# Kernel tuning notes

Measured on AMD Instinct MI355X. Metric: run time of the kernel, lower is better.

Reference implementation:

```python
import jax, jax.numpy as jnp
import numpy as np

B, S, D, F, E, K = 4, 2048, 768, 3072, 8, 2
LB_W, Z_W = 0.01, 0.001


def setup_inputs() -> dict:
    key = jax.random.key(0)
    ks = jax.random.split(key, 6)
    x = jax.random.normal(ks[0], (B, S, D), dtype=jnp.float32)
    Wr = jax.random.truncated_normal(ks[1], -2.0, 2.0, (D, E), dtype=jnp.float32) * 0.02
    W1 = jax.random.normal(ks[2], (E, D, F), dtype=jnp.float32) * (1.0 / np.sqrt(D))
    b1 = jnp.zeros((E, F), dtype=jnp.float32)
    W2 = jax.random.normal(ks[3], (E, F, D), dtype=jnp.float32) * (1.0 / np.sqrt(F))
    b2 = jnp.zeros((E, D), dtype=jnp.float32)
    return {"x": x, "Wr": Wr, "W1": W1, "b1": b1, "W2": W2, "b2": b2}


def reference(x, Wr, W1, b1, W2, b2):
    # Router
    router_logits = jnp.einsum('bsd,de->bse', x, Wr)            # [B,S,E]
    router_probs = jax.nn.softmax(router_logits, axis=-1)
    top_k_probs, top_k_idx = jax.lax.top_k(router_probs, K)     # [B,S,K]
    top_k_probs = top_k_probs / (jnp.sum(top_k_probs, axis=-1, keepdims=True) + 1e-8)

    # Auxiliary losses
    expert_usage = jnp.mean(router_probs, axis=(0, 1))          # [E]
    mean_usage = jnp.mean(expert_usage)
    var_usage = jnp.mean(jnp.square(expert_usage - mean_usage))
    lb_loss = var_usage / (mean_usage * mean_usage + 1e-8) * jnp.float32(E)
    z_loss = jnp.mean(jnp.square(jax.nn.logsumexp(router_logits, axis=-1)))

    # Combine weights per expert: sum over top-k slots assigned to expert e
    one_hot = jax.nn.one_hot(top_k_idx, E, dtype=x.dtype)       # [B,S,K,E]
    combine = jnp.sum(one_hot * top_k_probs[..., None], axis=2) # [B,S,E]

    # Expert FFNs (loop over fixed small E, vectorized over tokens)
    output = jnp.zeros_like(x)
    for e in range(E):
        h = jax.nn.gelu(jnp.einsum('bsd,df->bsf', x, W1[e]) + b1[e], approximate=False)
        y = jnp.einsum('bsf,fd->bsd', h, W2[e]) + b2[e]
        output = output + y * combine[..., e:e + 1]

    aux = {"load_balancing_loss": lb_loss * LB_W, "router_z_loss": z_loss * Z_W}
    return output, aux["load_balancing_loss"], aux["router_z_loss"]
```

## Files before the change

kernel.cpp:

```cpp
#include <hip/hip_runtime.h>
#include <cstdint>
#include <cstddef>

#define B_ 4
#define S_ 2048
#define D_ 768
#define F_ 3072
#define E_ 8
#define NTOK (B_*S_)
#define NASSIGN (NTOK*2)
#define RBLK 256
#define FBLK 32
#define MAXTILE 136

typedef unsigned short u16;
typedef __attribute__((ext_vector_type(8))) __bf16 bf16x8;
typedef __attribute__((ext_vector_type(4))) float f32x4;

__device__ __forceinline__ u16 f2bf(float f) {
    unsigned int u = __builtin_bit_cast(unsigned int, f);
    u += 0x7fffu + ((u >> 16) & 1u);
    return (u16)(u >> 16);
}

__device__ __forceinline__ void async16(const void* g, void* l) {
    __builtin_amdgcn_global_load_lds(
        (const __attribute__((address_space(1))) unsigned int*)g,
        (__attribute__((address_space(3))) unsigned int*)l, 16, 0, 0);
}

__device__ __forceinline__ float gelu_f(float v) {
    float z = v * 0.70710678f;
    float a = fabsf(z);
    float t = __builtin_amdgcn_rcpf(1.0f + 0.3275911f * a);
    float poly = t * (0.254829592f + t * (-0.284496736f + t * (1.421413741f +
                 t * (-1.453152027f + t * 1.061405429f))));
    float e = __expf(-z * z);
    float erf_z = copysignf(1.0f - poly * e, z);
    return 0.5f * v * (1.0f + erf_z);
}

__global__ void k_init(int* cursors) {
    int t = threadIdx.x;
    if (t < E_) cursors[t] = 0;
}

__global__ void k_cvt_x(const float* __restrict__ x, u16* __restrict__ xb) {
    int id = blockIdx.x * 256 + threadIdx.x;
    float4 v = ((const float4*)x)[id];
    ushort4 o;
    o.x = f2bf(v.x); o.y = f2bf(v.y); o.z = f2bf(v.z); o.w = f2bf(v.w);
    ((ushort4*)xb)[id] = o;
}

__global__ void k_tcvt(const float* __restrict__ in, u16* __restrict__ out, int R, int C) {
    __shared__ u16 t[32][33];
    int e = blockIdx.z;
    int c0 = blockIdx.x * 32, r0 = blockIdx.y * 32;
    int tx = threadIdx.x & 7;
    int ty = threadIdx.x >> 3;
    const float* ip = in + (size_t)e * R * C + (size_t)(r0 + ty) * C + c0 + tx * 4;
    float4 v = *(const float4*)ip;
    t[tx * 4 + 0][ty] = f2bf(v.x);
    t[tx * 4 + 1][ty] = f2bf(v.y);
    t[tx * 4 + 2][ty] = f2bf(v.z);
    t[tx * 4 + 3][ty] = f2bf(v.w);
    __syncthreads();
    u16* op = out + (size_t)e * C * R + (size_t)(c0 + ty) * R + r0 + tx * 4;
    ushort4 o;
    o.x = t[ty][tx * 4 + 0]; o.y = t[ty][tx * 4 + 1];
    o.z = t[ty][tx * 4 + 2]; o.w = t[ty][tx * 4 + 3];
    *(ushort4*)op = o;
}

__global__ __launch_bounds__(256) void k_router(
    const float* __restrict__ x, const float* __restrict__ Wr,
    float* __restrict__ usage_part, float* __restrict__ z_part,
    int* __restrict__ hist_part,
    int* __restrict__ tk_idx, float* __restrict__ tk_w)
{
    __shared__ float wrt[E_ * D_];
    __shared__ float s_usage[E_];
    __shared__ float s_z;
    __shared__ int   s_hist[E_];
    int tid = threadIdx.x;
    for (int i = tid; i < E_ * D_; i += 256) {
        int d = i >> 3, e = i & 7;
        wrt[e * D_ + d] = Wr[i];
    }
    if (tid < E_) { s_usage[tid] = 0.f; s_hist[tid] = 0; }
    if (tid == 0) s_z = 0.f;
    __syncthreads();

    int w = tid >> 6, lane = tid & 63;
    float u_acc[E_];
    #pragma unroll
    for (int e = 0; e < E_; e++) u_acc[e] = 0.f;
    float z_acc = 0.f;

    for (int it = 0; it < 8; it++) {
        int tok = blockIdx.x * 32 + it * 4 + w;
        float acc[E_];
        #pragma unroll
        for (int e = 0; e < E_; e++) acc[e] = 0.f;
        const float* xr = x + (size_t)tok * D_;
        for (int d = lane; d < D_; d += 64) {
            float xv = xr[d];
            #pragma unroll
            for (int e = 0; e < E_; e++) acc[e] += xv * wrt[e * D_ + d];
        }
        #pragma unroll
        for (int off = 32; off > 0; off >>= 1) {
            #pragma unroll
            for (int e = 0; e < E_; e++) acc[e] += __shfl_down(acc[e], off);
        }
        if (lane == 0) {
            float m = acc[0];
            #pragma unroll
            for (int e = 1; e < E_; e++) m = fmaxf(m, acc[e]);
            float p[E_], s = 0.f;
            #pragma unroll
            for (int e = 0; e < E_; e++) { p[e] = expf(acc[e] - m); s += p[e]; }
            float inv = 1.f / s;
            #pragma unroll
            for (int e = 0; e < E_; e++) { p[e] *= inv; u_acc[e] += p[e]; }
            float lse = m + logf(s);
            z_acc += lse * lse;
            int i1 = 0;
            for (int e = 1; e < E_; e++) if (p[e] > p[i1]) i1 = e;
            int i2 = -1;
            for (int e = 0; e < E_; e++) {
                if (e == i1) continue;
                if (i2 < 0 || p[e] > p[i2]) i2 = e;
            }
            float denom = p[i1] + p[i2] + 1e-8f;
            tk_idx[tok * 2 + 0] = i1; tk_idx[tok * 2 + 1] = i2;
            tk_w[tok * 2 + 0] = p[i1] / denom;
            tk_w[tok * 2 + 1] = p[i2] / denom;
            atomicAdd(&s_hist[i1], 1); atomicAdd(&s_hist[i2], 1);
        }
    }
    if (lane == 0) {
        #pragma unroll
        for (int e = 0; e < E_; e++) atomicAdd(&s_usage[e], u_acc[e]);
        atomicAdd(&s_z, z_acc);
    }
    __syncthreads();
    if (tid < E_) {
        usage_part[blockIdx.x * E_ + tid] = s_usage[tid];
        hist_part[blockIdx.x * E_ + tid]  = s_hist[tid];
    }
    if (tid == 0) z_part[blockIdx.x] = s_z;
}

__global__ __launch_bounds__(256) void k_finalize(
    const float* __restrict__ usage_part, const float* __restrict__ z_part,
    const int* __restrict__ hist_part,
    int* __restrict__ counts, int* __restrict__ offsets,
    int* __restrict__ tile_list,
    float* __restrict__ out_scalars)
{
    __shared__ float s_u[E_];
    __shared__ float s_z;
    __shared__ int   s_h[E_];
    int tid = threadIdx.x;
    if (tid < E_) { s_u[tid] = 0.f; s_h[tid] = 0; }
    if (tid == 0) s_z = 0.f;
    __syncthreads();

    float u[E_]; int h[E_];
    #pragma unroll
    for (int e = 0; e < E_; e++) { u[e] = usage_part[tid * E_ + e]; h[e] = hist_part[tid * E_ + e]; }
    float z = z_part[tid];
    #pragma unroll
    for (int off = 32; off > 0; off >>= 1) {
        #pragma unroll
        for (int e = 0; e < E_; e++) {
            u[e] += __shfl_down(u[e], off);
            h[e] += __shfl_down(h[e], off);
        }
        z += __shfl_down(z, off);
    }
    if ((tid & 63) == 0) {
        #pragma unroll
        for (int e = 0; e < E_; e++) { atomicAdd(&s_u[e], u[e]); atomicAdd(&s_h[e], h[e]); }
        atomicAdd(&s_z, z);
    }
    __syncthreads();
    if (tid == 0) {
        int o = 0, nt = 0;
        for (int e = 0; e < E_; e++) {
            int c = s_h[e];
            counts[e] = c; offsets[e] = o; o += c;
            for (int m0 = 0; m0 < c; m0 += 128) tile_list[1 + nt++] = (m0 << 8) | e;
        }
        tile_list[0] = nt;
        float uu[E_], mean = 0.f;
        for (int e = 0; e < E_; e++) { uu[e] = s_u[e] / (float)NTOK; mean += uu[e]; }
        mean /= (float)E_;
        float var = 0.f;
        for (int e = 0; e < E_; e++) { float d = uu[e] - mean; var += d * d; }
        var /= (float)E_;
        out_scalars[0] = var / (mean * mean + 1e-8f) * (float)E_ * 0.01f;
        out_scalars[1] = (s_z / (float)NTOK) * 0.001f;
    }
}

__global__ __launch_bounds__(256) void k_fill(
    const int* __restrict__ tk_idx, const float* __restrict__ tk_w,
    const int* __restrict__ offsets, int* __restrict__ cursors,
    int* __restrict__ assign_token, float* __restrict__ assign_weight)
{
    __shared__ int l_cnt[E_];
    __shared__ int l_base[E_];
    int tid = threadIdx.x;
    if (tid < E_) l_cnt[tid] = 0;
    __syncthreads();
    int t = blockIdx.x * 256 + tid;
    int e0 = tk_idx[t * 2 + 0], e1 = tk_idx[t * 2 + 1];
    int r0 = atomicAdd(&l_cnt[e0], 1);
    int r1 = atomicAdd(&l_cnt[e1], 1);
    __syncthreads();
    if (tid < E_) l_base[tid] = atomicAdd(&cursors[tid], l_cnt[tid]);
    __syncthreads();
    int row0 = offsets[e0] + l_base[e0] + r0;
    int row1 = offsets[e1] + l_base[e1] + r1;
    assign_token[row0] = t; assign_weight[row0] = tk_w[t * 2 + 0];
    assign_token[row1] = t; assign_weight[row1] = tk_w[t * 2 + 1];
}

__global__ __launch_bounds__(256) void k_gemm1(
    const u16* __restrict__ xb, const u16* __restrict__ w1t,
    const float* __restrict__ b1,
    const int* __restrict__ counts, const int* __restrict__ offsets,
    const int* __restrict__ tile_list,
    const int* __restrict__ assign_token, u16* __restrict__ h)
{
    int bid = blockIdx.x;
    int xcd = bid & 7;
    int j = bid >> 3;
    int nx = j / 17;
    int mt = xcd * 17 + (j % 17);
    int nt = tile_list[0];
    if (mt >= nt) return;
    int packed = tile_list[1 + mt];
    int e = packed & 0xff;
    int m0 = packed >> 8;
    int cnt = counts[e];
    int off = offsets[e];
    int n0 = nx * 128;

    __shared__ __align__(16) u16 SM[16384];
    char* smb = (char*)SM;

    int tid = threadIdx.x;
    int w = tid >> 6, lane = tid & 63;
    int rA = lane >> 2;
    int colk = ((lane & 3) ^ (rA & 3)) * 8;
    int r0 = (w * 2 + 0) * 16 + rA;
    int r1 = (w * 2 + 1) * 16 + rA;

    int c0b = __builtin_amdgcn_readfirstlane((w * 2 + 0) * 1024);
    int c1b = __builtin_amdgcn_readfirstlane((w * 2 + 1) * 1024);

    int g0 = m0 + r0; if (g0 > cnt - 1) g0 = cnt - 1;
    int g1 = m0 + r1; if (g1 > cnt - 1) g1 = cnt - 1;
    const u16* agp0 = xb + (size_t)assign_token[off + g0] * D_ + colk;
    const u16* agp1 = xb + (size_t)assign_token[off + g1] * D_ + colk;
    const u16* bgp0 = w1t + ((size_t)e * F_ + n0 + r0) * D_ + colk;
    const u16* bgp1 = w1t + ((size_t)e * F_ + n0 + r1) * D_ + colk;

    f32x4 acc[4][4];
    #pragma unroll
    for (int i = 0; i < 4; i++)
        #pragma unroll
        for (int j2 = 0; j2 < 4; j2++) acc[i][j2] = (f32x4){0.f, 0.f, 0.f, 0.f};

    int wm = (w >> 1) * 64, wn = (w & 1) * 64;
    int fm = lane & 15;
    int slot = ((lane >> 4) ^ (fm & 3)) * 8;

    #define STAGE1(buf, kk) do { \
        async16(agp0 + (kk), smb + (buf) * 8192 + c0b); \
        async16(agp1 + (kk), smb + (buf) * 8192 + c1b); \
        async16(bgp0 + (kk), smb + 16384 + (buf) * 8192 + c0b); \
        async16(bgp1 + (kk), smb + 16384 + (buf) * 8192 + c1b); \
    } while (0)
    #define COMPUTE1(buf) do { \
        const u16* Ab = SM + (buf) * 4096; \
        const u16* Bb = SM + 8192 + (buf) * 4096; \
        bf16x8 af[4], bfr[4]; \
        _Pragma("unroll") \
        for (int i = 0; i < 4; i++) af[i] = *(const bf16x8*)&Ab[(wm + i * 16 + fm) * 32 + slot]; \
        _Pragma("unroll") \
        for (int j2 = 0; j2 < 4; j2++) bfr[j2] = *(const bf16x8*)&Bb[(wn + j2 * 16 + fm) * 32 + slot]; \
        _Pragma("unroll") \
        for (int i = 0; i < 4; i++) \
            _Pragma("unroll") \
            for (int j2 = 0; j2 < 4; j2++) \
                acc[i][j2] = __builtin_amdgcn_mfma_f32_16x16x32_bf16(af[i], bfr[j2], acc[i][j2], 0, 0, 0); \
    } while (0)

    STAGE1(0, 0);
    __syncthreads();
    for (int kk = 0; kk < D_; kk += 64) {
        STAGE1(1, kk + 32);
        COMPUTE1(0);
        __syncthreads();
        if (kk + 64 < D_) STAGE1(0, kk + 64);
        COMPUTE1(1);
        __syncthreads();
    }
    #undef STAGE1
    #undef COMPUTE1

    int rbase = (lane >> 4) * 4;
    u16* tb = SM + w * 4096;
    float biasv[4];
    #pragma unroll
    for (int j2 = 0; j2 < 4; j2++) biasv[j2] = b1[e * F_ + n0 + wn + j2 * 16 + fm];
    #pragma unroll
    for (int i = 0; i < 4; i++)
        #pragma unroll
        for (int j2 = 0; j2 < 4; j2++)
            #pragma unroll
            for (int r = 0; r < 4; r++) {
                int m_l = i * 16 + rbase + r;
                int f_l = j2 * 16 + fm;
                u16 q = f2bf(gelu_f(acc[i][j2][r] + biasv[j2]));
                tb[m_l * 64 + ((((f_l >> 3) ^ (m_l & 7)) << 3) | (f_l & 7))] = q;
            }
    __syncthreads();
    #pragma unroll
    for (int s = 0; s < 8; s++) {
        int m_l = s * 8 + (lane >> 3);
        int c = lane & 7;
        uint4 vv = *(const uint4*)&tb[m_l * 64 + ((c ^ (m_l & 7)) << 3)];
        int m = m0 + wm + m_l;
        if (m < cnt)
            *(uint4*)&h[(size_t)(off + m) * F_ + n0 + wn + c * 8] = vv;
    }
}

__global__ __launch_bounds__(256) void k_gemm2(
    const u16* __restrict__ h, const u16* __restrict__ w2t,
    const float* __restrict__ b2,
    const int* __restrict__ counts, const int* __restrict__ offsets,
    const int* __restrict__ tile_list,
    const int* __restrict__ assign_token, const float* __restrict__ assign_weight,
    float* __restrict__ out)
{
    int bid = blockIdx.x;
    int xcd = bid & 7;
    int j = bid >> 3;
    int nx = j % 6;
    int mt = xcd * 17 + (j / 6);
    int nt = tile_list[0];
    if (mt >= nt) return;
    int packed = tile_list[1 + mt];
    int e = packed & 0xff;
    int m0 = packed >> 8;
    int cnt = counts[e];
    int off = offsets[e];
    int n0 = nx * 128;

    __shared__ __align__(16) u16 SM[16384];
    char* smb = (char*)SM;

    int tid = threadIdx.x;
    int w = tid >> 6, lane = tid & 63;
    int rA = lane >> 2;
    int colk = ((lane & 3) ^ (rA & 3)) * 8;
    int r0 = (w * 2 + 0) * 16 + rA;
    int r1 = (w * 2 + 1) * 16 + rA;

    int c0b = __builtin_amdgcn_readfirstlane((w * 2 + 0) * 1024);
    int c1b = __builtin_amdgcn_readfirstlane((w * 2 + 1) * 1024);

    const u16* agp0 = h + (size_t)(off + m0 + r0) * F_ + colk;
    const u16* agp1 = h + (size_t)(off + m0 + r1) * F_ + colk;
    const u16* bgp0 = w2t + ((size_t)e * D_ + n0 + r0) * F_ + colk;
    const u16* bgp1 = w2t + ((size_t)e * D_ + n0 + r1) * F_ + colk;

    f32x4 acc[4][4];
    #pragma unroll
    for (int i = 0; i < 4; i++)
        #pragma unroll
        for (int j2 = 0; j2 < 4; j2++) acc[i][j2] = (f32x4){0.f, 0.f, 0.f, 0.f};

    int wm = (w >> 1) * 64, wn = (w & 1) * 64;
    int fm = lane & 15;
    int slot = ((lane >> 4) ^ (fm & 3)) * 8;

    #define STAGE2(buf, kk) do { \
        async16(agp0 + (kk), smb + (buf) * 8192 + c0b); \
        async16(agp1 + (kk), smb + (buf) * 8192 + c1b); \
        async16(bgp0 + (kk), smb + 16384 + (buf) * 8192 + c0b); \
        async16(bgp1 + (kk), smb + 16384 + (buf) * 8192 + c1b); \
    } while (0)
    #define COMPUTE2(buf) do { \
        const u16* Ab = SM + (buf) * 4096; \
        const u16* Bb = SM + 8192 + (buf) * 4096; \
        bf16x8 af[4], bfr[4]; \
        _Pragma("unroll") \
        for (int i = 0; i < 4; i++) af[i] = *(const bf16x8*)&Ab[(wm + i * 16 + fm) * 32 + slot]; \
        _Pragma("unroll") \
        for (int j2 = 0; j2 < 4; j2++) bfr[j2] = *(const bf16x8*)&Bb[(wn + j2 * 16 + fm) * 32 + slot]; \
        _Pragma("unroll") \
        for (int i = 0; i < 4; i++) \
            _Pragma("unroll") \
            for (int j2 = 0; j2 < 4; j2++) \
                acc[i][j2] = __builtin_amdgcn_mfma_f32_16x16x32_bf16(af[i], bfr[j2], acc[i][j2], 0, 0, 0); \
    } while (0)

    STAGE2(0, 0);
    __syncthreads();
    for (int kk = 0; kk < F_; kk += 64) {
        STAGE2(1, kk + 32);
        COMPUTE2(0);
        __syncthreads();
        if (kk + 64 < F_) STAGE2(0, kk + 64);
        COMPUTE2(1);
        __syncthreads();
    }
    #undef STAGE2
    #undef COMPUTE2

    int rbase = (lane >> 4) * 4;
    float biasv[4];
    #pragma unroll
    for (int j2 = 0; j2 < 4; j2++) biasv[j2] = b2[e * D_ + n0 + wn + j2 * 16 + fm];
    #pragma unroll
    for (int i = 0; i < 4; i++)
        #pragma unroll
        for (int r = 0; r < 4; r++) {
            int m = m0 + wm + i * 16 + rbase + r;
            if (m < cnt) {
                int t = assign_token[off + m];
                float wg = assign_weight[off + m];
                float* orow = out + (size_t)t * D_ + n0 + wn + fm;
                #pragma unroll
                for (int j2 = 0; j2 < 4; j2++)
                    unsafeAtomicAdd(orow + j2 * 16, (acc[i][j2][r] + biasv[j2]) * wg);
            }
        }
}

extern "C" void kernel_launch(void* const* d_in, const int* in_sizes, int n_in,
                              void* d_out, int out_size, void* d_ws, size_t ws_size,
                              hipStream_t stream)
{
    const float* x  = (const float*)d_in[0];
    const float* Wr = (const float*)d_in[1];
    const float* W1 = (const float*)d_in[2];
    const float* b1 = (const float*)d_in[3];
    const float* W2 = (const float*)d_in[4];
    const float* b2 = (const float*)d_in[5];
    float* out = (float*)d_out;

    char* base = (char*)d_ws;
    size_t o = 0;
    auto alloc = [&](size_t bytes) {
        char* r = base + o;
        o += (bytes + 255) & ~(size_t)255;
        return r;
    };
    int*   counts        = (int*)  alloc(E_ * 4);
    int*   cursors       = (int*)  alloc(E_ * 4);
    int*   offsets       = (int*)  alloc(E_ * 4);
    int*   tile_list     = (int*)  alloc(256 * 4);
    float* usage_part    = (float*)alloc((size_t)RBLK * E_ * 4);
    float* z_part        = (float*)alloc((size_t)RBLK * 4);
    int*   hist_part     = (int*)  alloc((size_t)RBLK * E_ * 4);
    int*   tk_idx        = (int*)  alloc((size_t)NTOK * 2 * 4);
    float* tk_w          = (float*)alloc((size_t)NTOK * 2 * 4);
    int*   assign_token  = (int*)  alloc((size_t)NASSIGN * 4);
    float* assign_weight = (float*)alloc((size_t)NASSIGN * 4);
    u16*   xb            = (u16*)  alloc((size_t)NTOK * D_ * 2);
    u16*   w1t           = (u16*)  alloc((size_t)E_ * F_ * D_ * 2);
    u16*   w2t           = (u16*)  alloc((size_t)E_ * D_ * F_ * 2);
    u16*   hbuf          = (u16*)  alloc((size_t)(NASSIGN + 128) * F_ * 2);

    hipMemsetAsync(d_out, 0, (size_t)out_size * 4, stream);
    k_init<<<dim3(1), dim3(64), 0, stream>>>(cursors);
    k_cvt_x<<<dim3(NTOK * D_ / 1024), dim3(256), 0, stream>>>(x, xb);
    k_tcvt<<<dim3(F_ / 32, D_ / 32, E_), dim3(256), 0, stream>>>(W1, w1t, D_, F_);
    k_tcvt<<<dim3(D_ / 32, F_ / 32, E_), dim3(256), 0, stream>>>(W2, w2t, F_, D_);
    k_router<<<dim3(RBLK), dim3(256), 0, stream>>>(x, Wr, usage_part, z_part, hist_part, tk_idx, tk_w);
    k_finalize<<<dim3(1), dim3(256), 0, stream>>>(usage_part, z_part, hist_part, counts, offsets,
                                                  tile_list, out + (size_t)NTOK * D_);
    k_fill<<<dim3(FBLK), dim3(256), 0, stream>>>(tk_idx, tk_w, offsets, cursors, assign_token, assign_weight);
    k_gemm1<<<dim3(8 * 17 * (F_ / 128)), dim3(256), 0, stream>>>(xb, w1t, b1, counts, offsets, tile_list,
                                                                 assign_token, hbuf);
    k_gemm2<<<dim3(8 * 17 * (D_ / 128)), dim3(256), 0, stream>>>(hbuf, w2t, b2, counts, offsets, tile_list,
                                                                 assign_token, assign_weight, out);
}
```

Before: 607.2 us.

## Load MFMA fragments directly from global memory, dropping LDS staging in expert GEMMs

Both expert GEMM kernels stop staging A and B tiles through shared memory with async global-to-LDS loads and barriers. Each lane now loads its bf16x8 MFMA fragments straight from global memory into registers, double-buffered in registers across k-steps. This removes LDS traffic and __syncthreads, but each wave reloads operand rows that other waves share, so global and L2 traffic rises and loads become strided 16-byte accesses rather than cooperative tile loads.

```diff
diff --git a/kernel.cpp b/kernel.cpp
--- a/kernel.cpp
+++ b/kernel.cpp
@@ -21,12 +21,6 @@
     unsigned int u = __builtin_bit_cast(unsigned int, f);
     u += 0x7fffu + ((u >> 16) & 1u);
     return (u16)(u >> 16);
-}
-
-__device__ __forceinline__ void async16(const void* g, void* l) {
-    __builtin_amdgcn_global_load_lds(
-        (const __attribute__((address_space(1))) unsigned int*)g,
-        (__attribute__((address_space(3))) unsigned int*)l, 16, 0, 0);
 }
 
 __device__ __forceinline__ float gelu_f(float v) {
@@ -229,6 +223,20 @@
     assign_token[row1] = t; assign_weight[row1] = tk_w[t * 2 + 1];
 }
 
+#define LOAD_FRAGS(av, bv, kk) do { \
+    _Pragma("unroll") \
+    for (int i = 0; i < 4; i++) av[i] = *(const bf16x8*)(arow[i] + (kk)); \
+    _Pragma("unroll") \
+    for (int j = 0; j < 4; j++) bv[j] = *(const bf16x8*)(brow[j] + (kk)); \
+} while (0)
+#define DO_MFMA(av, bv) do { \
+    _Pragma("unroll") \
+    for (int i = 0; i < 4; i++) \
+        _Pragma("unroll") \
+        for (int j = 0; j < 4; j++) \
+            acc[i][j] = __builtin_amdgcn_mfma_f32_16x16x32_bf16(av[i], bv[j], acc[i][j], 0, 0, 0); \
+} while (0)
+
 __global__ __launch_bounds__(256) void k_gemm1(
     const u16* __restrict__ xb, const u16* __restrict__ w1t,
     const float* __restrict__ b1,
@@ -251,68 +259,38 @@
     int n0 = nx * 128;
 
     __shared__ __align__(16) u16 SM[16384];
-    char* smb = (char*)SM;
 
     int tid = threadIdx.x;
     int w = tid >> 6, lane = tid & 63;
-    int rA = lane >> 2;
-    int colk = ((lane & 3) ^ (rA & 3)) * 8;
-    int r0 = (w * 2 + 0) * 16 + rA;
-    int r1 = (w * 2 + 1) * 16 + rA;
-
-    int c0b = __builtin_amdgcn_readfirstlane((w * 2 + 0) * 1024);
-    int c1b = __builtin_amdgcn_readfirstlane((w * 2 + 1) * 1024);
-
-    int g0 = m0 + r0; if (g0 > cnt - 1) g0 = cnt - 1;
-    int g1 = m0 + r1; if (g1 > cnt - 1) g1 = cnt - 1;
-    const u16* agp0 = xb + (size_t)assign_token[off + g0] * D_ + colk;
-    const u16* agp1 = xb + (size_t)assign_token[off + g1] * D_ + colk;
-    const u16* bgp0 = w1t + ((size_t)e * F_ + n0 + r0) * D_ + colk;
-    const u16* bgp1 = w1t + ((size_t)e * F_ + n0 + r1) * D_ + colk;
-
-    f32x4 acc[4][4];
-    #pragma unroll
-    for (int i = 0; i < 4; i++)
-        #pragma unroll
-        for (int j2 = 0; j2 < 4; j2++) acc[i][j2] = (f32x4){0.f, 0.f, 0.f, 0.f};
-
     int wm = (w >> 1) * 64, wn = (w & 1) * 64;
     int fm = lane & 15;
-    int slot = ((lane >> 4) ^ (fm & 3)) * 8;
-
-    #define STAGE1(buf, kk) do { \
-        async16(agp0 + (kk), smb + (buf) * 8192 + c0b); \
-        async16(agp1 + (kk), smb + (buf) * 8192 + c1b); \
-        async16(bgp0 + (kk), smb + 16384 + (buf) * 8192 + c0b); \
-        async16(bgp1 + (kk), smb + 16384 + (buf) * 8192 + c1b); \
-    } while (0)
-    #define COMPUTE1(buf) do { \
-        const u16* Ab = SM + (buf) * 4096; \
-        const u16* Bb = SM + 8192 + (buf) * 4096; \
-        bf16x8 af[4], bfr[4]; \
-        _Pragma("unroll") \
-        for (int i = 0; i < 4; i++) af[i] = *(const bf16x8*)&Ab[(wm + i * 16 + fm) * 32 + slot]; \
-        _Pragma("unroll") \
-        for (int j2 = 0; j2 < 4; j2++) bfr[j2] = *(const bf16x8*)&Bb[(wn + j2 * 16 + fm) * 32 + slot]; \
-        _Pragma("unroll") \
-        for (int i = 0; i < 4; i++) \
-            _Pragma("unroll") \
-            for (int j2 = 0; j2 < 4; j2++) \
-                acc[i][j2] = __builtin_amdgcn_mfma_f32_16x16x32_bf16(af[i], bfr[j2], acc[i][j2], 0, 0, 0); \
-    } while (0)
-
-    STAGE1(0, 0);
-    __syncthreads();
+    int kq = (lane >> 4) * 8;
+
+    const u16* arow[4];
+    const u16* brow[4];
+    #pragma unroll
+    for (int i = 0; i < 4; i++) {
+        int g = m0 + wm + i * 16 + fm; if (g > cnt - 1) g = cnt - 1;
+        arow[i] = xb + (size_t)assign_token[off + g] * D_ + kq;
+    }
+    #pragma unroll
+    for (int j2 = 0; j2 < 4; j2++)
+        brow[j2] = w1t + ((size_t)e * F_ + n0 + wn + j2 * 16 + fm) * D_ + kq;
+
+    f32x4 acc[4][4];
+    #pragma unroll
+    for (int i = 0; i < 4; i++)
+        #pragma unroll
+        for (int j2 = 0; j2 < 4; j2++) acc[i][j2] = (f32x4){0.f, 0.f, 0.f, 0.f};
+
+    bf16x8 a0[4], b0v[4], a1[4], b1v[4];
+    LOAD_FRAGS(a0, b0v, 0);
     for (int kk = 0; kk < D_; kk += 64) {
-        STAGE1(1, kk + 32);
-        COMPUTE1(0);
-        __syncthreads();
-        if (kk + 64 < D_) STAGE1(0, kk + 64);
-        COMPUTE1(1);
-        __syncthreads();
-    }
-    #undef STAGE1
-    #undef COMPUTE1
+        LOAD_FRAGS(a1, b1v, kk + 32);
+        DO_MFMA(a0, b0v);
+        if (kk + 64 < D_) LOAD_FRAGS(a0, b0v, kk + 64);
+        DO_MFMA(a1, b1v);
+    }
 
     int rbase = (lane >> 4) * 4;
     u16* tb = SM + w * 4096;
@@ -364,67 +342,35 @@
     int off = offsets[e];
     int n0 = nx * 128;
 
-    __shared__ __align__(16) u16 SM[16384];
-    char* smb = (char*)SM;
-
     int tid = threadIdx.x;
     int w = tid >> 6, lane = tid & 63;
-    int rA = lane >> 2;
-    int colk = ((lane & 3) ^ (rA & 3)) * 8;
-    int r0 = (w * 2 + 0) * 16 + rA;
-    int r1 = (w * 2 + 1) * 16 + rA;
-
-    int c0b = __builtin_amdgcn_readfirstlane((w * 2 + 0) * 1024);
-    int c1b = __builtin_amdgcn_readfirstlane((w * 2 + 1) * 1024);
-
-    const u16* agp0 = h + (size_t)(off + m0 + r0) * F_ + colk;
-    const u16* agp1 = h + (size_t)(off + m0 + r1) * F_ + colk;
-    const u16* bgp0 = w2t + ((size_t)e * D_ + n0 + r0) * F_ + colk;
-    const u16* bgp1 = w2t + ((size_t)e * D_ + n0 + r1) * F_ + colk;
-
-    f32x4 acc[4][4];
-    #pragma unroll
-    for (int i = 0; i < 4; i++)
-        #pragma unroll
-        for (int j2 = 0; j2 < 4; j2++) acc[i][j2] = (f32x4){0.f, 0.f, 0.f, 0.f};
-
     int wm = (w >> 1) * 64, wn = (w & 1) * 64;
     int fm = lane & 15;
-    int slot = ((lane >> 4) ^ (fm & 3)) * 8;
-
-    #define STAGE2(buf, kk) do { \
-        async16(agp0 + (kk), smb + (buf) * 8192 + c0b); \
-        async16(agp1 + (kk), smb + (buf) * 8192 + c1b); \
-        async16(bgp0 + (kk), smb + 16384 + (buf) * 8192 + c0b); \
-        async16(bgp1 + (kk), smb + 16384 + (buf) * 8192 + c1b); \
-    } while (0)
-    #define COMPUTE2(buf) do { \
-        const u16* Ab = SM + (buf) * 4096; \
-        const u16* Bb = SM + 8192 + (buf) * 4096; \
-        bf16x8 af[4], bfr[4]; \
-        _Pragma("unroll") \
-        for (int i = 0; i < 4; i++) af[i] = *(const bf16x8*)&Ab[(wm + i * 16 + fm) * 32 + slot]; \
-        _Pragma("unroll") \
-        for (int j2 = 0; j2 < 4; j2++) bfr[j2] = *(const bf16x8*)&Bb[(wn + j2 * 16 + fm) * 32 + slot]; \
-        _Pragma("unroll") \
-        for (int i = 0; i < 4; i++) \
-            _Pragma("unroll") \
-            for (int j2 = 0; j2 < 4; j2++) \
-                acc[i][j2] = __builtin_amdgcn_mfma_f32_16x16x32_bf16(af[i], bfr[j2], acc[i][j2], 0, 0, 0); \
-    } while (0)
-
-    STAGE2(0, 0);
-    __syncthreads();
+    int kq = (lane >> 4) * 8;
+
+    const u16* arow[4];
+    const u16* brow[4];
+    #pragma unroll
+    for (int i = 0; i < 4; i++)
+        arow[i] = h + (size_t)(off + m0 + wm + i * 16 + fm) * F_ + kq;
+    #pragma unroll
+    for (int j2 = 0; j2 < 4; j2++)
+        brow[j2] = w2t + ((size_t)e * D_ + n0 + wn + j2 * 16 + fm) * F_ + kq;
+
+    f32x4 acc[4][4];
+    #pragma unroll
+    for (int i = 0; i < 4; i++)
+        #pragma unroll
+        for (int j2 = 0; j2 < 4; j2++) acc[i][j2] = (f32x4){0.f, 0.f, 0.f, 0.f};
+
+    bf16x8 a0[4], b0v[4], a1[4], b1v[4];
+    LOAD_FRAGS(a0, b0v, 0);
     for (int kk = 0; kk < F_; kk += 64) {
-        STAGE2(1, kk + 32);
-        COMPUTE2(0);
-        __syncthreads();
-        if (kk + 64 < F_) STAGE2(0, kk + 64);
-        COMPUTE2(1);
-        __syncthreads();
-    }
-    #undef STAGE2
-    #undef COMPUTE2
+        LOAD_FRAGS(a1, b1v, kk + 32);
+        DO_MFMA(a0, b0v);
+        if (kk + 64 < F_) LOAD_FRAGS(a0, b0v, kk + 64);
+        DO_MFMA(a1, b1v);
+    }
 
     int rbase = (lane >> 4) * 4;
     float biasv[4];
```

Result: slower. 953.1 us (+57.0%).
